# Kernel optimization log

Hardware: AMD Instinct MI355X
Metric: run time of the kernel (lower is better)

The kernel has to match this reference:

```python
import jax, jax.numpy as jnp
import numpy as np

B, C, H, W, K = 32, 64, 64, 64, 1024
COMMITMENT_COST = 0.25


def setup_inputs() -> dict:
    key = jax.random.key(0)
    k1, k2, k3, k4 = jax.random.split(key, 4)
    input1 = jax.random.normal(k1, (B, C, H, W), dtype=jnp.float32)
    input2_KL = jax.random.normal(k2, (B,), dtype=jnp.float32)
    x_tilde = jax.random.randint(k3, (B * H * W,), 0, K)  # channel-corrupted indices
    # codebook init: uniform(-1/K, 1/K) as in nn.Embedding init in the module
    weight = jax.random.uniform(k4, (K, C), dtype=jnp.float32, minval=-1.0 / K, maxval=1.0 / K)
    return {"input1": input1, "input2_KL": input2_KL, "weight": weight, "x_tilde": x_tilde}


def reference(input1, input2_KL, weight, x_tilde):
    # [B,C,H,W] -> [B,H,W,C]
    x = jnp.transpose(input1, (0, 2, 3, 1))
    input_shape = x.shape
    flat = x.reshape(-1, weight.shape[1])  # [N, D]
    distances = (jnp.sum(flat * flat, axis=1, keepdims=True)
                 + jnp.sum(weight * weight, axis=1)
                 - 2.0 * jnp.matmul(flat, weight.T))
    idx = jnp.argmin(distances, axis=1)  # [N]
    encodings = jax.nn.one_hot(idx, K, dtype=jnp.float32)  # scatter one-hot
    # channel noise: one_hot(corrupted) - one_hot(clean)
    noise = jax.nn.one_hot(x_tilde, K, dtype=jnp.float32) - encodings
    encodings = encodings + noise
    # recover: [N,K] @ [K,D] -> [N,D]
    quantized = jnp.matmul(encodings, weight).reshape(input_shape)
    e_latent_loss = jnp.mean((jax.lax.stop_gradient(quantized) - x) ** 2)
    q_latent_loss = jnp.mean((quantized - jax.lax.stop_gradient(x)) ** 2)
    loss = q_latent_loss + COMMITMENT_COST * e_latent_loss
    # straight-through estimator
    quantized = x + jax.lax.stop_gradient(quantized - x)
    return loss, input2_KL, jnp.transpose(quantized, (0, 3, 1, 2)), encodings
```

## Files before the change

### kernel.cpp

```cpp
#include <hip/hip_runtime.h>

constexpr int B_ = 32, C_ = 64, H_ = 64, W_ = 64, K_ = 1024;
constexpr int NTOT = B_ * C_ * H_ * W_;
constexpr int NSP  = B_ * H_ * W_;
constexpr int OFF_Q   = 33;
constexpr int OFF_ENC = OFF_Q + NTOT;
constexpr long long ENC_ELEMS = (long long)NSP * K_;
constexpr int ENC_HEAD = 15;
constexpr int ENC_NQ = (int)((ENC_ELEMS - ENC_HEAD - 1) / 4);
constexpr int ENC_BLOCKS = (ENC_NQ + 255) / 256;

constexpr int MAIN_BLOCKS  = NSP / 64;
constexpr int TOTAL_BLOCKS = MAIN_BLOCKS + ENC_BLOCKS;

typedef float v4f __attribute__((ext_vector_type(4)));

__global__ __launch_bounds__(256) void vq_fused(const float* __restrict__ input1,
                                                const int*   __restrict__ x_tilde,
                                                const float* __restrict__ weight,
                                                float* __restrict__ out,
                                                float* __restrict__ acc) {
    const int bid = blockIdx.x;
    if (bid >= MAIN_BLOCKS) {
        const int b  = bid - MAIN_BLOCKS;
        const int qi = b * 256 + threadIdx.x;
        if (qi >= ENC_NQ) return;
        const int t0 = x_tilde[b];
        const int t1 = x_tilde[(b + 1 < NSP) ? b + 1 : NSP - 1];
        const int col0 = ENC_HEAD + (threadIdx.x << 2);
        v4f v;
        #pragma unroll
        for (int j = 0; j < 4; ++j) {
            const int col = col0 + j;
            ((float*)&v)[j] = (col < 1024) ? ((t0 == col) ? 1.f : 0.f)
                                           : ((t1 == col - 1024) ? 1.f : 0.f);
        }
        *reinterpret_cast<v4f*>(out + OFF_ENC + ENC_HEAD + (qi << 2)) = v;
        return;
    }

    const int tid = threadIdx.x;
    const int n   = bid * 64 + (tid & 63);
    const int cq  = tid >> 6;
    const int b   = n >> 12;
    const int hw  = n & 4095;
    const int t   = x_tilde[n];
    const float* __restrict__ wrow = weight + (t << 6) + (cq << 4);
    const float* __restrict__ xin  = input1 + (b << 18) + (cq << 16) + hw;
    float* __restrict__ qout = out + OFF_Q + (b << 18) + (cq << 16) + hw;

    const float4 w0 = *reinterpret_cast<const float4*>(wrow);
    const float4 w1 = *reinterpret_cast<const float4*>(wrow + 4);
    const float4 w2 = *reinterpret_cast<const float4*>(wrow + 8);
    const float4 w3 = *reinterpret_cast<const float4*>(wrow + 12);
    const float wv[16] = {w0.x, w0.y, w0.z, w0.w, w1.x, w1.y, w1.z, w1.w,
                          w2.x, w2.y, w2.z, w2.w, w3.x, w3.y, w3.z, w3.w};
    float local = 0.f;
    #pragma unroll
    for (int j = 0; j < 16; ++j) {
        const float x = xin[j << 12];
        const float d = wv[j] - x;
        qout[j << 12] = x + d;
        local += d * d;
    }

    for (int o = 32; o > 0; o >>= 1) local += __shfl_down(local, o);
    __shared__ float sm[4];
    const int lane = tid & 63, wid = tid >> 6;
    if (lane == 0) sm[wid] = local;
    __syncthreads();
    if (tid == 0) {
        atomicAdd(acc, sm[0] + sm[1] + sm[2] + sm[3]);
    }
}

__global__ void vq_fin(const int* __restrict__ x_tilde,
                       const float* __restrict__ acc,
                       const float* __restrict__ kl,
                       float* __restrict__ out) {
    const int t = threadIdx.x;
    if (t < 32) out[1 + t] = kl[t];
    if (t == 32) out[0] = 1.25f * (*acc) / (float)NTOT;
    if (t == 33) {
        const int t0 = x_tilde[0];
        #pragma unroll
        for (int j = 0; j < ENC_HEAD; ++j)
            out[OFF_ENC + j] = (t0 == j) ? 1.f : 0.f;
        const int tl = x_tilde[NSP - 1];
        out[OFF_ENC + (int)ENC_ELEMS - 1] = (tl == 1023) ? 1.f : 0.f;
    }
}

extern "C" void kernel_launch(void* const* d_in, const int* in_sizes, int n_in,
                              void* d_out, int out_size, void* d_ws, size_t ws_size,
                              hipStream_t stream) {
    const float* input1 = (const float*)d_in[0];
    const float* kl     = (const float*)d_in[1];
    const float* weight = (const float*)d_in[2];
    const int*   x_til  = (const int*)d_in[3];
    float* out = (float*)d_out;
    float* acc = (float*)d_ws;

    (void)hipMemsetAsync(acc, 0, sizeof(float), stream);

    vq_fused<<<TOTAL_BLOCKS, 256, 0, stream>>>(input1, x_til, weight, out, acc);
    vq_fin<<<1, 64, 0, stream>>>(x_til, acc, kl, out);
}
```

Before: 132.5 us.

## Replace atomic loss accumulation with per-block partials and widen encoding stores

Each main block now writes its partial squared-error sum to its own workspace slot instead of doing a global atomicAdd. The finalize kernel reduces the 2048 partials with 256 threads, which lets the memset launch be dropped. Separately, each encoding-writer thread now emits eight floats as two vector stores, halving the number of encoding blocks. The change trades atomic contention and an extra launch for a small extra reduction in the finalize kernel.

New measurement: 134.6 us. Within noise of the previous version (+1.7%).

```diff
diff --git a/kernel.cpp b/kernel.cpp
--- a/kernel.cpp
+++ b/kernel.cpp
@@ -7,8 +7,8 @@
 constexpr int OFF_ENC = OFF_Q + NTOT;
 constexpr long long ENC_ELEMS = (long long)NSP * K_;
 constexpr int ENC_HEAD = 15;
-constexpr int ENC_NQ = (int)((ENC_ELEMS - ENC_HEAD - 1) / 4);
-constexpr int ENC_BLOCKS = (ENC_NQ + 255) / 256;
+constexpr int ENC_N8 = (int)((ENC_ELEMS - ENC_HEAD - 1) / 8);
+constexpr int ENC_BLOCKS = (ENC_N8 + 255) / 256;
 
 constexpr int MAIN_BLOCKS  = NSP / 64;
 constexpr int TOTAL_BLOCKS = MAIN_BLOCKS + ENC_BLOCKS;
@@ -19,23 +19,30 @@
                                                 const int*   __restrict__ x_tilde,
                                                 const float* __restrict__ weight,
                                                 float* __restrict__ out,
-                                                float* __restrict__ acc) {
+                                                float* __restrict__ ws) {
     const int bid = blockIdx.x;
     if (bid >= MAIN_BLOCKS) {
-        const int b  = bid - MAIN_BLOCKS;
-        const int qi = b * 256 + threadIdx.x;
-        if (qi >= ENC_NQ) return;
-        const int t0 = x_tilde[b];
-        const int t1 = x_tilde[(b + 1 < NSP) ? b + 1 : NSP - 1];
-        const int col0 = ENC_HEAD + (threadIdx.x << 2);
-        v4f v;
+        const int eb = bid - MAIN_BLOCKS;
+        const int g  = eb * 256 + threadIdx.x;
+        if (g >= ENC_N8) return;
+        const int r0 = eb << 1;
+        const int t0 = x_tilde[r0];
+        const int t1 = x_tilde[r0 + 1];
+        const int t2 = x_tilde[(r0 + 2 < NSP) ? r0 + 2 : NSP - 1];
+        const int c0 = ENC_HEAD + (threadIdx.x << 3);
+        v4f va, vb;
         #pragma unroll
-        for (int j = 0; j < 4; ++j) {
-            const int col = col0 + j;
-            ((float*)&v)[j] = (col < 1024) ? ((t0 == col) ? 1.f : 0.f)
-                                           : ((t1 == col - 1024) ? 1.f : 0.f);
+        for (int j = 0; j < 8; ++j) {
+            const int e   = c0 + j;
+            const int sel = e >> 10;
+            const int col = e & 1023;
+            const int t   = (sel == 0) ? t0 : ((sel == 1) ? t1 : t2);
+            const float f = (t == col) ? 1.f : 0.f;
+            if (j < 4) ((float*)&va)[j] = f; else ((float*)&vb)[j - 4] = f;
         }
-        *reinterpret_cast<v4f*>(out + OFF_ENC + ENC_HEAD + (qi << 2)) = v;
+        float* p = out + OFF_ENC + ENC_HEAD + (g << 3);
+        *reinterpret_cast<v4f*>(p)     = va;
+        *reinterpret_cast<v4f*>(p + 4) = vb;
         return;
     }
 
@@ -70,18 +77,25 @@
     if (lane == 0) sm[wid] = local;
     __syncthreads();
     if (tid == 0) {
-        atomicAdd(acc, sm[0] + sm[1] + sm[2] + sm[3]);
+        ws[bid] = sm[0] + sm[1] + sm[2] + sm[3];
     }
 }
 
-__global__ void vq_fin(const int* __restrict__ x_tilde,
-                       const float* __restrict__ acc,
-                       const float* __restrict__ kl,
-                       float* __restrict__ out) {
-    const int t = threadIdx.x;
-    if (t < 32) out[1 + t] = kl[t];
-    if (t == 32) out[0] = 1.25f * (*acc) / (float)NTOT;
-    if (t == 33) {
+__global__ __launch_bounds__(256) void vq_fin(const int* __restrict__ x_tilde,
+                                              const float* __restrict__ ws,
+                                              const float* __restrict__ kl,
+                                              float* __restrict__ out) {
+    const int tid = threadIdx.x;
+    float local = 0.f;
+    #pragma unroll
+    for (int k = 0; k < 8; ++k) local += ws[tid + (k << 8)];
+    for (int o = 32; o > 0; o >>= 1) local += __shfl_down(local, o);
+    __shared__ float sm[4];
+    if ((tid & 63) == 0) sm[tid >> 6] = local;
+    __syncthreads();
+    if (tid == 0) out[0] = 1.25f * (sm[0] + sm[1] + sm[2] + sm[3]) / (float)NTOT;
+    if (tid >= 64 && tid < 96) out[1 + tid - 64] = kl[tid - 64];
+    if (tid == 96) {
         const int t0 = x_tilde[0];
         #pragma unroll
         for (int j = 0; j < ENC_HEAD; ++j)
@@ -99,10 +113,8 @@
     const float* weight = (const float*)d_in[2];
     const int*   x_til  = (const int*)d_in[3];
     float* out = (float*)d_out;
-    float* acc = (float*)d_ws;
+    float* ws  = (float*)d_ws;
 
-    (void)hipMemsetAsync(acc, 0, sizeof(float), stream);
-
-    vq_fused<<<TOTAL_BLOCKS, 256, 0, stream>>>(input1, x_til, weight, out, acc);
-    vq_fin<<<1, 64, 0, stream>>>(x_til, acc, kl, out);
+    vq_fused<<<TOTAL_BLOCKS, 256, 0, stream>>>(input1, x_til, weight, out, ws);
+    vq_fin<<<1, 256, 0, stream>>>(x_til, ws, kl, out);
 }
```

## Replace atomic loss accumulation with per-block partials and schedule encoding blocks first

Applied to the files above, without the earlier changes.

Each main block now writes its partial squared-error sum to its own workspace slot instead of doing an atomicAdd. The final kernel reduces all 2048 partials with a 256-thread block, which removes the memset launch and the atomic contention. The block order is also swapped so the large one-hot encoding write blocks are dispatched before the quantize blocks. This costs a slightly heavier finalize kernel.

Result: faster. 122.5 us (-7.5%).

```diff
diff --git a/kernel.cpp b/kernel.cpp
--- a/kernel.cpp
+++ b/kernel.cpp
@@ -11,7 +11,7 @@
 constexpr int ENC_BLOCKS = (ENC_NQ + 255) / 256;
 
 constexpr int MAIN_BLOCKS  = NSP / 64;
-constexpr int TOTAL_BLOCKS = MAIN_BLOCKS + ENC_BLOCKS;
+constexpr int TOTAL_BLOCKS = ENC_BLOCKS + MAIN_BLOCKS;
 
 typedef float v4f __attribute__((ext_vector_type(4)));
 
@@ -19,10 +19,10 @@
                                                 const int*   __restrict__ x_tilde,
                                                 const float* __restrict__ weight,
                                                 float* __restrict__ out,
-                                                float* __restrict__ acc) {
+                                                float* __restrict__ ws) {
     const int bid = blockIdx.x;
-    if (bid >= MAIN_BLOCKS) {
-        const int b  = bid - MAIN_BLOCKS;
+    if (bid < ENC_BLOCKS) {
+        const int b  = bid;
         const int qi = b * 256 + threadIdx.x;
         if (qi >= ENC_NQ) return;
         const int t0 = x_tilde[b];
@@ -39,8 +39,9 @@
         return;
     }
 
+    const int mq  = bid - ENC_BLOCKS;
     const int tid = threadIdx.x;
-    const int n   = bid * 64 + (tid & 63);
+    const int n   = mq * 64 + (tid & 63);
     const int cq  = tid >> 6;
     const int b   = n >> 12;
     const int hw  = n & 4095;
@@ -70,18 +71,25 @@
     if (lane == 0) sm[wid] = local;
     __syncthreads();
     if (tid == 0) {
-        atomicAdd(acc, sm[0] + sm[1] + sm[2] + sm[3]);
+        ws[mq] = sm[0] + sm[1] + sm[2] + sm[3];
     }
 }
 
-__global__ void vq_fin(const int* __restrict__ x_tilde,
-                       const float* __restrict__ acc,
-                       const float* __restrict__ kl,
-                       float* __restrict__ out) {
-    const int t = threadIdx.x;
-    if (t < 32) out[1 + t] = kl[t];
-    if (t == 32) out[0] = 1.25f * (*acc) / (float)NTOT;
-    if (t == 33) {
+__global__ __launch_bounds__(256) void vq_fin(const int* __restrict__ x_tilde,
+                                              const float* __restrict__ ws,
+                                              const float* __restrict__ kl,
+                                              float* __restrict__ out) {
+    const int tid = threadIdx.x;
+    float local = 0.f;
+    #pragma unroll
+    for (int k = 0; k < 8; ++k) local += ws[tid + (k << 8)];
+    for (int o = 32; o > 0; o >>= 1) local += __shfl_down(local, o);
+    __shared__ float sm[4];
+    if ((tid & 63) == 0) sm[tid >> 6] = local;
+    __syncthreads();
+    if (tid == 0) out[0] = 1.25f * (sm[0] + sm[1] + sm[2] + sm[3]) / (float)NTOT;
+    if (tid >= 64 && tid < 96) out[1 + tid - 64] = kl[tid - 64];
+    if (tid == 96) {
         const int t0 = x_tilde[0];
         #pragma unroll
         for (int j = 0; j < ENC_HEAD; ++j)
@@ -99,10 +107,8 @@
     const float* weight = (const float*)d_in[2];
     const int*   x_til  = (const int*)d_in[3];
     float* out = (float*)d_out;
-    float* acc = (float*)d_ws;
+    float* ws  = (float*)d_ws;
 
-    (void)hipMemsetAsync(acc, 0, sizeof(float), stream);
-
-    vq_fused<<<TOTAL_BLOCKS, 256, 0, stream>>>(input1, x_til, weight, out, acc);
-    vq_fin<<<1, 64, 0, stream>>>(x_til, acc, kl, out);
+    vq_fused<<<TOTAL_BLOCKS, 256, 0, stream>>>(input1, x_til, weight, out, ws);
+    vq_fin<<<1, 256, 0, stream>>>(x_til, ws, kl, out);
 }
```
